# Kernel tuning notes

Hardware: AMD Instinct MI355X
Metric: run time of the kernel (lower is better)

Reference implementation:

```python
import jax, jax.numpy as jnp
import numpy as np

DN = ('NCHW', 'OIHW', 'NCHW')


def conv(x, w, s, p):
    return jax.lax.conv_general_dilated(x, w, (s, s), [(p, p), (p, p)], dimension_numbers=DN)


def batchnorm(x, g, b, eps=1e-5):
    # torch BatchNorm2d in training mode: biased batch stats over (N,H,W)
    mu = jnp.mean(x, (0, 2, 3), keepdims=True)
    var = jnp.var(x, (0, 2, 3), keepdims=True)
    return (x - mu) * jax.lax.rsqrt(var + eps) * g.reshape(1, -1, 1, 1) + b.reshape(1, -1, 1, 1)


def pconv(x, mask, W, b, s, p, gb, act):
    # PartialConvLayer.forward
    k = W.shape[-1]
    y = conv(x * mask, W, s, p)
    mc = conv(mask, jnp.ones((1, 1, k, k), x.dtype), s, p)  # all-ones mask conv (frozen)
    zero = mc == 0
    msum = jnp.where(zero, 1.0, mc)
    if b is not None:
        bias = b.reshape(1, -1, 1, 1)
        y = (y - bias) / msum + bias
    else:
        y = y / msum
    y = jnp.where(zero, 0.0, y)
    new_mask = jnp.where(zero, 0.0, 1.0).astype(x.dtype)
    if gb is not None:
        y = batchnorm(y, gb[0], gb[1])
    if act == 'relu':
        y = jax.nn.relu(y)
    elif act == 'leaky':
        y = jnp.where(y >= 0, y, 0.2 * y)
    return y, new_mask


def nlm(mask, feat, h2):
    # Vectorized batch_NLM: Nadaraya-Watson estimator between miss and bkg pixels.
    # Equivalent to the original triple loop: for each miss pixel i,
    #   out[i] = sum_j exp(-||x_i-x_j||^2/h^2) x_j / sum_j exp(-...)   over bkg j.
    # Subtracting the per-row min distance before exp is mathematically identical
    # (the factor cancels in the ratio) and numerically stable.
    bs, C, H, W = feat.shape
    N = H * W
    x = feat.transpose(0, 2, 3, 1).reshape(bs, N, C)
    bkg = mask.reshape(bs, N) > 0.5
    sq = jnp.sum(x * x, -1)  # [bs,N]
    D = jnp.maximum(sq[:, :, None] + sq[:, None, :] - 2.0 * jnp.einsum('bic,bjc->bij', x, x), 0.0)
    Dm = jnp.where(bkg[:, None, :], D, jnp.inf)
    dmin = jnp.min(Dm, -1, keepdims=True)
    w = jnp.where(bkg[:, None, :], jnp.exp(-(D - dmin) / h2), 0.0)
    avg = jnp.einsum('bij,bjc->bic', w, x) / jnp.sum(w, -1, keepdims=True)
    out = jnp.where(bkg[:, :, None], x, avg)  # only miss pixels are replaced
    return out.reshape(bs, H, W, C).transpose(0, 3, 1, 2)


def up2(x):
    return jnp.repeat(jnp.repeat(x, 2, axis=2), 2, axis=3)


def forward(input_x, mask, enc1_W, enc2_W, enc3_W, enc4_W, dec4_W, dec3_W, dec2_W, dec1_W, dec1_b,
            enc2_g, enc2_b, enc3_g, enc3_b, enc4_g, enc4_b,
            dec4_g, dec4_b, dec3_g, dec3_b, dec2_g, dec2_b):
    H_GAUSS2 = 25.0  # h_gaussian = 5
    h0, m0 = input_x, mask
    h1, m1 = pconv(h0, m0, enc1_W, None, 2, 3, None, 'relu')                 # down-7, bn=False
    h2, m2 = pconv(h1, m1, enc2_W, None, 2, 2, (enc2_g, enc2_b), 'relu')     # down-5
    # NLM feature swapping at layer 2 (torch code detaches -> stop_gradient)
    h2 = jax.lax.stop_gradient(nlm(m2, h2, H_GAUSS2))
    buffer_swapped = h2
    h3, m3 = pconv(h2, m2, enc3_W, None, 2, 1, (enc3_g, enc3_b), 'relu')     # down-3
    h4, m4 = pconv(h3, m3, enc4_W, None, 2, 1, (enc4_g, enc4_b), 'relu')     # down-3

    out, omask = h4, m4
    out, omask = up2(out), up2(omask)
    out, omask = pconv(jnp.concatenate([out, h3], 1), omask, dec4_W, None, 1, 1, (dec4_g, dec4_b), 'leaky')
    out, omask = up2(out), up2(omask)
    out, omask = pconv(jnp.concatenate([out, buffer_swapped], 1), omask, dec3_W, None, 1, 1, (dec3_g, dec3_b), 'leaky')
    out, omask = up2(out), up2(omask)
    out, omask = pconv(jnp.concatenate([out, h1], 1), omask, dec2_W, None, 1, 1, (dec2_g, dec2_b), 'leaky')
    out, omask = up2(out), up2(omask)
    out, omask = pconv(jnp.concatenate([out, h0], 1), omask, dec1_W, dec1_b, 1, 1, None, 'none')  # bn=False, bias, no act
    return out


def setup_inputs() -> dict:
    key = jax.random.key(0)
    ks = jax.random.split(key, 12)

    def kaiming(k, shape):
        fan_in = shape[1] * shape[2] * shape[3]
        return jax.random.normal(k, shape, jnp.float32) * np.float32(np.sqrt(2.0 / fan_in))

    bs = 8
    input_x = jax.random.normal(ks[0], (bs, 128, 144, 144), jnp.float32)
    # mask: 1 = background (valid), 0 = missing. Hole large enough to survive two downsamples.
    mask = jnp.ones((bs, 1, 144, 144), jnp.float32).at[:, :, 40:96, 40:96].set(0.0)

    inp = {
        'input_x': input_x,
        'mask': mask,
        'enc1_W': kaiming(ks[1], (256, 128, 7, 7)),
        'enc2_W': kaiming(ks[2], (512, 256, 5, 5)),
        'enc3_W': kaiming(ks[3], (512, 512, 3, 3)),
        'enc4_W': kaiming(ks[4], (512, 512, 3, 3)),
        'dec4_W': kaiming(ks[5], (512, 1024, 3, 3)),
        'dec3_W': kaiming(ks[6], (512, 1024, 3, 3)),
        'dec2_W': kaiming(ks[7], (256, 768, 3, 3)),
        'dec1_W': kaiming(ks[8], (128, 384, 3, 3)),
        'dec1_b': jnp.zeros((128,), jnp.float32),
    }
    for name, c in [('enc2', 512), ('enc3', 512), ('enc4', 512), ('dec4', 512), ('dec3', 512), ('dec2', 256)]:
        inp[name + '_g'] = jnp.ones((c,), jnp.float32)
        inp[name + '_b'] = jnp.zeros((c,), jnp.float32)
    return inp


def reference(input_x, mask, enc1_W, enc2_W, enc3_W, enc4_W, dec4_W, dec3_W, dec2_W, dec1_W, dec1_b,
              enc2_g, enc2_b, enc3_g, enc3_b, enc4_g, enc4_b,
              dec4_g, dec4_b, dec3_g, dec3_b, dec2_g, dec2_b):
    return forward(input_x, mask, enc1_W, enc2_W, enc3_W, enc4_W, dec4_W, dec3_W, dec2_W, dec1_W, dec1_b,
                   enc2_g, enc2_b, enc3_g, enc3_b, enc4_g, enc4_b,
                   dec4_g, dec4_b, dec3_g, dec3_b, dec2_g, dec2_b)
```

## Files before the change

kernel.cpp:

```cpp
#include <hip/hip_runtime.h>
#include <math.h>

#define ACT_NONE 0
#define ACT_RELU 1
#define ACT_LEAKY 2

#define EPI_F32 0
#define EPI_PAIR_RELU 1
#define EPI_F32_BIAS 2

typedef __attribute__((ext_vector_type(8))) short short8;
typedef __attribute__((ext_vector_type(8))) __bf16 bf16x8;
typedef __attribute__((ext_vector_type(4))) float f32x4;
typedef __attribute__((ext_vector_type(4))) unsigned uint4v;

__device__ __forceinline__ float actf(float y, int act) {
    if (act == ACT_RELU)  return y > 0.f ? y : 0.f;
    if (act == ACT_LEAKY) return y >= 0.f ? y : 0.2f * y;
    return y;
}

__device__ __forceinline__ unsigned f2bf_rne(float f) {
    unsigned u = __float_as_uint(f);
    return (u + 0x7FFFu + ((u >> 16) & 1u)) >> 16;
}
__device__ __forceinline__ float bf2f(unsigned h) { return __uint_as_float(h << 16); }
__device__ __forceinline__ unsigned splitpack(float f) {
    unsigned hi = f2bf_rne(f);
    float r = f - bf2f(hi);
    unsigned lo = f2bf_rne(r);
    return (hi & 0xFFFFu) | (lo << 16);
}

__device__ __forceinline__ f32x4 mfma16(short8 a, short8 b, f32x4 c) {
    return __builtin_amdgcn_mfma_f32_16x16x32_bf16(
        __builtin_bit_cast(bf16x8, a), __builtin_bit_cast(bf16x8, b), c, 0, 0, 0);
}

template<int K, int S, bool MHALF>
__global__ void maskconv_kernel(const float* __restrict__ M, int HM, int WM,
                                float* __restrict__ mc, float* __restrict__ nm,
                                int N, int Hin, int Win, int Hout, int Wout) {
    constexpr int P = (K - 1) / 2;
    int idx = blockIdx.x * blockDim.x + threadIdx.x;
    int total = N * Hout * Wout;
    if (idx >= total) return;
    int wo = idx % Wout;
    int t  = idx / Wout;
    int ho = t % Hout;
    int n  = t / Hout;
    float s = 0.f;
    for (int kh = 0; kh < K; ++kh) {
        int ih = ho * S - P + kh;
        if ((unsigned)ih >= (unsigned)Hin) continue;
        const float* mrow = M + ((size_t)n * HM + (MHALF ? (ih >> 1) : ih)) * WM;
        for (int kw = 0; kw < K; ++kw) {
            int iw = wo * S - P + kw;
            if ((unsigned)iw < (unsigned)Win)
                s += mrow[MHALF ? (iw >> 1) : iw];
// ... 7 lines not shown
                           short* __restrict__ Wlo, int Cout, int Cin, int Ksz,
                           size_t total) {
    size_t idx = (size_t)blockIdx.x * blockDim.x + threadIdx.x;
    if (idx >= total) return;
    int j = (int)(idx & 7);
    int lane = (int)((idx >> 3) & 63);
    size_t r = idx >> 9;
    int COB = Cout >> 4, KB = Cin >> 5;
    int cob = (int)(r % COB); r /= COB;
    int kb = (int)(r % KB);
    int tap = (int)(r / KB);
    int co = cob * 16 + (lane & 15);
    int ci = kb * 32 + (lane >> 4) * 8 + j;
    float f = W[((size_t)co * Cin + ci) * Ksz + tap];
    unsigned hi = f2bf_rne(f);
    float rr = f - bf2f(hi);
    unsigned lo = f2bf_rne(rr);
    Whi[idx] = (short)hi;
    Wlo[idx] = (short)lo;
}

template<int K, int S, int TH, int TW, int NFW, bool AF32, int EPI>
__global__ __launch_bounds__(512) void conv_enc(
    const void* __restrict__ Asrc, int Cin, int Hin, int Win,
    const float* __restrict__ M,
    const short* __restrict__ Whi, const short* __restrict__ Wlo,
    const float* __restrict__ mc, const float* __restrict__ bias,
    void* __restrict__ outp,
    int Hout, int Wout, int Cout, int TX)
{
    static_assert(S == 2, "parity layout assumes stride 2");
    constexpr int P = (K - 1) / 2;
    constexpr int HH  = (TH - 1) * S + K;
    constexpr int HWC = (TW - 1) * S + K;
    constexpr int PXC = HH * HWC;
    static_assert(PXC <= 512, "one halo pixel per thread");
    constexpr int PW  = (HWC + 1) / 2;
    constexpr int PXC2 = HH * PW * 2;
    __shared__ __align__(16) unsigned BH[4 * PXC2 * 4];
    __shared__ __align__(16) unsigned BL[4 * PXC2 * 4];

    const int t    = threadIdx.x;
    const int lane = t & 63;
    const int wv   = t >> 6;
    const int wm   = wv >> 1;
    const int wn   = wv & 1;
    const int img  = blockIdx.z;
    const int coB  = blockIdx.y * 256;
    const int tile = blockIdx.x;
    const int ty   = tile / TX, tx = tile - ty * TX;
    const int oy0  = ty * TH, ox0 = tx * TW;
    const int KB   = Cin >> 5;
    const int COB  = Cout >> 4;
    const size_t HW = (size_t)Hin * Win;
    const int g  = lane >> 4;
    const int pl = lane & 15;

    bool sel = false;
    size_t base = 0;
    int qq = 0;
    if (t < PXC) {
        const int r = t / HWC, c = t - r * HWC;
        qq = r * PW + (c >> 1) + (c & 1) * (HH * PW);
        const int iy = oy0 * S - P + r;
        const int ix = ox0 * S - P + c;
        if ((unsigned)iy < (unsigned)Hin && (unsigned)ix < (unsigned)Win) {
            if (M[(size_t)img * HW + (size_t)iy * Win + ix] != 0.f) {
                sel = true;
                base = (size_t)img * Cin * HW + (size_t)iy * Win + ix;
            }
        }
    }

    unsigned vr[4][8];
    auto prefetch = [&](int kb) {
#pragma unroll
        for (int gg = 0; gg < 4; ++gg) {
            const int c0 = kb * 32 + gg * 8;
#pragma unroll
            for (int j = 0; j < 8; ++j) vr[gg][j] = 0u;
            if (sel) {
                const unsigned* s = (const unsigned*)Asrc + base + (size_t)c0 * HW;
#pragma unroll
                for (int j = 0; j < 8; ++j) vr[gg][j] = s[(size_t)j * HW];
            }
        }
    };

    f32x4 acc[4][NFW] = {};
    if (t < PXC) prefetch(0);

#pragma unroll 1
    for (int kb = 0; kb < KB; ++kb) {
        if (t < PXC) {
#pragma unroll
            for (int gg = 0; gg < 4; ++gg) {
                unsigned v[8];
#pragma unroll
                for (int j = 0; j < 8; ++j) {
                    v[j] = vr[gg][j];
                    if (AF32) v[j] = splitpack(__uint_as_float(v[j]));
                }
                uint4v hd, ld;
#pragma unroll
                for (int j = 0; j < 4; ++j) {
                    hd[j] = (v[2 * j] & 0xFFFFu) | (v[2 * j + 1] << 16);
                    ld[j] = (v[2 * j] >> 16) | (v[2 * j + 1] & 0xFFFF0000u);
                }
                *(uint4v*)&BH[(gg * PXC2 + qq) * 4] = hd;
                *(uint4v*)&BL[(gg * PXC2 + qq) * 4] = ld;
            }
        }
        __syncthreads();
        if (t < PXC && kb + 1 < KB) prefetch(kb + 1);

#pragma unroll 1
        for (int kh = 0; kh < K; ++kh)
#pragma unroll 1
        for (int kw = 0; kw < K; ++kw) {
            const int tap = kh * K + kw;
            const size_t wb = (((size_t)tap * KB + kb) * COB + (coB >> 4) + wm * 4) * 512
                            + (size_t)lane * 8;
            short8 ah[4], al[4];
#pragma unroll
            for (int fm = 0; fm < 4; ++fm) {
                ah[fm] = *(const short8*)(Whi + wb + (size_t)fm * 512);
                al[fm] = *(const short8*)(Wlo + wb + (size_t)fm * 512);
            }
#pragma unroll
            for (int fn = 0; fn < NFW; ++fn) {
                const int pxf = (wn * NFW + fn) * 16 + pl;
                const int oy = pxf / TW, ox = pxf - oy * TW;
                const int q2 = (oy * S + kh) * PW + ox + (kw >> 1) + (kw & 1) * (HH * PW);
                short8 bh = *(const short8*)&BH[(g * PXC2 + q2) * 4];
                short8 bl = *(const short8*)&BL[(g * PXC2 + q2) * 4];
#pragma unroll
                for (int fm = 0; fm < 4; ++fm) {
                    acc[fm][fn] = mfma16(ah[fm], bh, acc[fm][fn]);
                    acc[fm][fn] = mfma16(al[fm], bh, acc[fm][fn]);
                    acc[fm][fn] = mfma16(ah[fm], bl, acc[fm][fn]);
                }
            }
        }
        __syncthreads();
    }

    const int Npix = Hout * Wout;
    const float* mcb = mc + (size_t)img * Npix;
#pragma unroll
    for (int fm = 0; fm < 4; ++fm)
#pragma unroll
    for (int fn = 0; fn < NFW; ++fn) {
        const int co = coB + (wm * 4 + fm) * 16 + (lane >> 4) * 4;
        const int pxf = (wn * NFW + fn) * 16 + (lane & 15);
        const int oy = pxf / TW, ox = pxf - oy * TW;
        const int gy = oy0 + oy, gx = ox0 + ox;
        if (gy >= Hout || gx >= Wout) continue;
        const float m = mcb[(size_t)gy * Wout + gx];
        f32x4 a = acc[fm][fn];
#pragma unroll
        for (int r = 0; r < 4; ++r) {
            float y = a[r];
            if (EPI == EPI_F32_BIAS) {
                const float bv = bias[co + r];
                y = (m == 0.f) ? 0.f : (y - bv) / m + bv;
            } else {
                y = (m == 0.f) ? 0.f : y / m;
            }
            const size_t oidx = ((size_t)img * Cout + co + r) * Npix + (size_t)gy * Wout + gx;
            if (EPI == EPI_PAIR_RELU) {
                y = y > 0.f ? y : 0.f;
                ((unsigned*)outp)[oidx] = splitpack(y);
            } else {
                ((float*)outp)[oidx] = y;
            }
        }
    }
}

template<int TH, int TW, int NFW, bool BF32, int EPI>
__global__ __launch_bounds__(512) void conv3x3(
    const void* __restrict__ Asrc, int CA, int HA, int WA,
    const void* __restrict__ Bsrc, int CB,
    const float* __restrict__ M,
    const short* __restrict__ Whi, const short* __restrict__ Wlo,
    const float* __restrict__ mc, const float* __restrict__ bias,
    void* __restrict__ outp,
    int Hout, int Wout, int Cout, int TX)
{
    constexpr int HALO_H = TH + 2, HALO_W = TW + 2, HALO = HALO_H * HALO_W;
    constexpr int NPIX = TH * TW;
    constexpr int SITER = (HALO + 127) / 128;
    static_assert(NPIX == 32 * NFW, "tile must be exactly 32*NFW pixels");
    __shared__ __align__(16) unsigned BH[4 * HALO * 4];
    __shared__ __align__(16) unsigned BL[4 * HALO * 4];

    const int t    = threadIdx.x;
    const int lane = t & 63;
    const int wv   = t >> 6;
    const int wm   = wv >> 1;
    const int wn   = wv & 1;
    const int img  = blockIdx.z;
    const int coB  = blockIdx.y * 128;
    const int tile = blockIdx.x;
    const int ty   = tile / TX;
    const int tx   = tile - ty * TX;
    const int oy0  = ty * TH, ox0 = tx * TW;
    const int Cin  = CA + CB;
    const int KB   = Cin >> 5;
    const int COB  = Cout >> 4;
    const int WM   = Wout >> 1;
    const size_t HWA = (size_t)HA * WA;
    const size_t HWB = (size_t)Hout * Wout;

    const int sg = t >> 7;
    const int st = t & 127;
    const int g  = lane >> 4;
    const int pl = lane & 15;

    bool ssel[SITER];
    size_t sA[SITER], sB[SITER];
#pragma unroll
    for (int i = 0; i < SITER; ++i) {
        ssel[i] = false; sA[i] = 0; sB[i] = 0;
        const int q = st + i * 128;
        if (q < HALO) {
            const int hy = q / HALO_W, hx = q - hy * HALO_W;
            const int iy = oy0 - 1 + hy, ix = ox0 - 1 + hx;
            if ((unsigned)iy < (unsigned)Hout && (unsigned)ix < (unsigned)Wout) {
                if (M[((size_t)img * (Hout >> 1) + (iy >> 1)) * WM + (ix >> 1)] != 0.f) {
                    ssel[i] = true;
                    sA[i] = (size_t)img * CA * HWA + (size_t)(iy >> 1) * WA + (ix >> 1);
                    sB[i] = (size_t)img * CB * HWB + (size_t)iy * Wout + ix;
                }
            }
        }
    }

    unsigned vr[SITER][8];
    auto prefetch = [&](int kb) {
        const int c = kb * 32 + sg * 8;
#pragma unroll
        for (int i = 0; i < SITER; ++i) {
            const int q = st + i * 128;
#pragma unroll
            for (int j = 0; j < 8; ++j) vr[i][j] = 0u;
            if (q < HALO && ssel[i]) {
                if (c < CA) {
                    const unsigned* s = (const unsigned*)Asrc + sA[i] + (size_t)c * HWA;
#pragma unroll
                    for (int j = 0; j < 8; ++j) vr[i][j] = s[(size_t)j * HWA];
                } else {
                    const unsigned* s = (const unsigned*)Bsrc + sB[i] + (size_t)(c - CA) * HWB;
#pragma unroll
                    for (int j = 0; j < 8; ++j) vr[i][j] = s[(size_t)j * HWB];
                }
            }
        }
    };

    f32x4 acc[2][NFW] = {};
    const size_t wstride = (size_t)KB * COB * 512;
    prefetch(0);

#pragma unroll 1
    for (int kb = 0; kb < KB; ++kb) {
        const bool isB = (kb * 32 + sg * 8) >= CA;
#pragma unroll
        for (int i = 0; i < SITER; ++i) {
            const int q = st + i * 128;
            if (q < HALO) {
                unsigned v[8];
#pragma unroll
                for (int j = 0; j < 8; ++j) {
                    v[j] = vr[i][j];
                    if (BF32 && isB) v[j] = splitpack(__uint_as_float(v[j]));
                }
                uint4v hd, ld;
#pragma unroll
                for (int j = 0; j < 4; ++j) {
                    hd[j] = (v[2 * j] & 0xFFFFu) | (v[2 * j + 1] << 16);
                    ld[j] = (v[2 * j] >> 16) | (v[2 * j + 1] & 0xFFFF0000u);
                }
                *(uint4v*)&BH[(sg * HALO + q) * 4] = hd;
                *(uint4v*)&BL[(sg * HALO + q) * 4] = ld;
            }
        }
        __syncthreads();
        if (kb + 1 < KB) prefetch(kb + 1);

        size_t wb = ((size_t)kb * COB + (coB >> 4) + wm * 2) * 512 + (size_t)lane * 8;
#pragma unroll 1
        for (int tap = 0; tap < 9; ++tap) {
            const int dh = tap / 3, dw = tap - dh * 3;
            short8 ah0 = *(const short8*)(Whi + wb);
            short8 ah1 = *(const short8*)(Whi + wb + 512);
            short8 al0 = *(const short8*)(Wlo + wb);
            short8 al1 = *(const short8*)(Wlo + wb + 512);
#pragma unroll
            for (int fn = 0; fn < NFW; ++fn) {
                const int pxf = (wn * NFW + fn) * 16 + pl;
                const int oy = pxf / TW, ox = pxf - oy * TW;
                const int hpx = (oy + dh) * HALO_W + (ox + dw);
                short8 bh = *(const short8*)&BH[(g * HALO + hpx) * 4];
                short8 bl = *(const short8*)&BL[(g * HALO + hpx) * 4];
                acc[0][fn] = mfma16(ah0, bh, acc[0][fn]);
                acc[1][fn] = mfma16(ah1, bh, acc[1][fn]);
                acc[0][fn] = mfma16(al0, bh, acc[0][fn]);
                acc[1][fn] = mfma16(al1, bh, acc[1][fn]);
                acc[0][fn] = mfma16(ah0, bl, acc[0][fn]);
                acc[1][fn] = mfma16(ah1, bl, acc[1][fn]);
            }
            wb += wstride;
        }
        __syncthreads();
    }

    const float* mcb = mc + (size_t)img * HWB;
#pragma unroll
    for (int fm = 0; fm < 2; ++fm)
#pragma unroll
    for (int fn = 0; fn < NFW; ++fn) {
        const int co = coB + (wm * 2 + fm) * 16 + (lane >> 4) * 4;
        const int pxf = (wn * NFW + fn) * 16 + (lane & 15);
        const int oy = pxf / TW, ox = pxf - oy * TW;
        const int gy = oy0 + oy, gx = ox0 + ox;
        if (gy >= Hout || gx >= Wout) continue;
        const float m = mcb[(size_t)gy * Wout + gx];
// ... 20 lines not shown
    double s = 0.0, s2 = 0.0;
    const int tot = N * HW;
    for (int i = threadIdx.x; i < tot; i += blockDim.x) {
        int n = i / HW, hw = i - n * HW;
        float v = y[((size_t)n * C + c) * HW + hw];
        s += v;
        s2 += (double)v * v;
    }
    __shared__ double sh[256], sh2[256];
    sh[threadIdx.x] = s; sh2[threadIdx.x] = s2;
    __syncthreads();
    for (int o = 128; o > 0; o >>= 1) {
        if (threadIdx.x < o) { sh[threadIdx.x] += sh[threadIdx.x + o]; sh2[threadIdx.x] += sh2[threadIdx.x + o]; }
        __syncthreads();
    }
    if (threadIdx.x == 0) {
        double mu = sh[0] / tot;
        double var = sh2[0] / tot - mu * mu;
        mean[c] = (float)mu;
        istd[c] = (float)(1.0 / sqrt(var + 1e-5));
    }
}

__global__ void bn_apply_pair(const float* __restrict__ y,
                              const float* __restrict__ mean, const float* __restrict__ istd,
                              const float* __restrict__ g, const float* __restrict__ b,
                              unsigned* __restrict__ pout, float* __restrict__ fout,
                              int C, int HW, int total, int act) {
    int idx = blockIdx.x * blockDim.x + threadIdx.x;
    if (idx >= total) return;
    int c = (idx / HW) % C;
    float v = (y[idx] - mean[c]) * istd[c] * g[c] + b[c];
    v = actf(v, act);
    pout[idx] = splitpack(v);
    if (fout) fout[idx] = v;
}

#define NLM_C 512
#define NLM_N 1296
#define NLM_MAXM 256
#define NLM_RT 16
#define NLM_KB1 16
#define NLM_KB2 41
#define NLM_PFRAG (NLM_KB1 * NLM_RT * 512)
#define NLM_WFRAG (NLM_KB2 * NLM_RT * 512)

__global__ __launch_bounds__(256) void nlm_trans(const float* __restrict__ h2f,
                                                 unsigned* __restrict__ xTp) {
    __shared__ float tile[32][33];
    const int b = blockIdx.z;
    const int j0 = blockIdx.x * 32, c0 = blockIdx.y * 32;
    const int tx = threadIdx.x & 31, ty = threadIdx.x >> 5;
    for (int cc = ty; cc < 32; cc += 8) {
        const int j = j0 + tx;
        tile[cc][tx] = (j < NLM_N) ? h2f[((size_t)b * NLM_C + c0 + cc) * NLM_N + j] : 0.f;
    }
    __syncthreads();
    for (int jj = ty; jj < 32; jj += 8) {
// ... 166 lines not shown
            lsum += w;
        }
        const unsigned u = splitpack(w);
        const int kb = j >> 5, kg = (j & 31) >> 3, jj = j & 7;
        const int lane = kg * 16 + lr;
        const size_t f = (size_t)img * NLM_WFRAG
                       + ((size_t)(kb * NLM_RT + rt) * 64 + lane) * 8 + jj;
        W2hi[f] = (short)(u & 0xFFFFu);
        W2lo[f] = (short)(u >> 16);
    }
    red[tid] = lsum;
    __syncthreads();
    for (int o = 128; o > 0; o >>= 1) {
        if (tid < o) red[tid] += red[tid + o];
        __syncthreads();
    }
    if (tid == 0) sumw[img * NLM_MAXM + i] = red[0];
}

__global__ __launch_bounds__(512) void nlm_gemm2(
    const unsigned* __restrict__ xTp, const short* __restrict__ W2hi,
    const short* __restrict__ W2lo, const int* __restrict__ cnt,
    const float* __restrict__ sumw, const int* __restrict__ list,
    unsigned* __restrict__ out) {
    const int img = blockIdx.z, mt = blockIdx.y, ct = blockIdx.x;
    const int cN = cnt[img] < NLM_MAXM ? cnt[img] : NLM_MAXM;
    if (mt * 128 >= cN) return;
    __shared__ __align__(16) unsigned BH[4 * 128 * 4];
    __shared__ __align__(16) unsigned BL[4 * 128 * 4];
    const int t = threadIdx.x, lane = t & 63, wv = t >> 6, wm = wv >> 1, wn = wv & 1;
    const int c0 = ct * 128;
    const int sc = t & 127, sg = t >> 7;
    f32x4 acc[2][4] = {};
#pragma unroll 1
    for (int kb = 0; kb < NLM_KB2; ++kb) {
        unsigned v[8];
#pragma unroll
        for (int jj = 0; jj < 8; ++jj) {
            const int j = kb * 32 + sg * 8 + jj;
            v[jj] = (j < NLM_N)
                  ? xTp[((size_t)img * NLM_N + j) * NLM_C + c0 + sc] : 0u;
        }
        uint4v hd, ld;
#pragma unroll
        for (int jj = 0; jj < 4; ++jj) {
            hd[jj] = (v[2 * jj] & 0xFFFFu) | (v[2 * jj + 1] << 16);
            ld[jj] = (v[2 * jj] >> 16) | (v[2 * jj + 1] & 0xFFFF0000u);
// ... 14 lines not shown
            short8 bh = *(const short8*)&BH[(g * 128 + px) * 4];
            short8 bl = *(const short8*)&BL[(g * 128 + px) * 4];
            acc[0][fn] = mfma16(ah0, bh, acc[0][fn]);
            acc[1][fn] = mfma16(ah1, bh, acc[1][fn]);
            acc[0][fn] = mfma16(al0, bh, acc[0][fn]);
            acc[1][fn] = mfma16(al1, bh, acc[1][fn]);
            acc[0][fn] = mfma16(ah0, bl, acc[0][fn]);
            acc[1][fn] = mfma16(ah1, bl, acc[1][fn]);
        }
        __syncthreads();
    }
#pragma unroll
    for (int fm = 0; fm < 2; ++fm)
#pragma unroll
    for (int fn = 0; fn < 4; ++fn) {
        const int row = mt * 128 + (wm * 2 + fm) * 16 + (lane >> 4) * 4;
        const int c = c0 + wn * 64 + fn * 16 + (lane & 15);
        f32x4 a = acc[fm][fn];
#pragma unroll
        for (int r = 0; r < 4; ++r) {
            const int ri = row + r;
            if (ri < cN) {
                const float y = a[r] / sumw[img * NLM_MAXM + ri];
                out[((size_t)img * NLM_C + c) * NLM_N + list[img * NLM_MAXM + ri]]
                    = splitpack(y);
            }
        }
    }
}

extern "C" void kernel_launch(void* const* d_in, const int* in_sizes, int n_in,
                              void* d_out, int out_size, void* d_ws, size_t ws_size,
                              hipStream_t stream) {
    const float* x0    = (const float*)d_in[0];
    const float* m0    = (const float*)d_in[1];
    const float* Wsrc[8] = {
        (const float*)d_in[2], (const float*)d_in[3], (const float*)d_in[4],
        (const float*)d_in[5], (const float*)d_in[6], (const float*)d_in[7],
        (const float*)d_in[8], (const float*)d_in[9]
    };
    const float* dec1b = (const float*)d_in[10];
    const float* enc2g = (const float*)d_in[11];
    const float* enc2b = (const float*)d_in[12];
    const float* enc3g = (const float*)d_in[13];
    const float* enc3b = (const float*)d_in[14];
    const float* enc4g = (const float*)d_in[15];
    const float* enc4b = (const float*)d_in[16];
    const float* dec4g = (const float*)d_in[17];
    const float* dec4b = (const float*)d_in[18];
    const float* dec3g = (const float*)d_in[19];
    const float* dec3b = (const float*)d_in[20];
    const float* dec2g = (const float*)d_in[21];
    const float* dec2b = (const float*)d_in[22];
    float* outp = (float*)d_out;

    const int N = 8;
    float* ws = (float*)d_ws;
    size_t off = 0;
    auto alloc = [&](size_t nf) {
        size_t o = off;
        off += ((nf + 63) / 64) * 64;
        return ws + o;
    };

    unsigned* h1pair  = (unsigned*)alloc(10616832);
    unsigned* h2spair = (unsigned*)alloc(5308416);
    unsigned* h3pair  = (unsigned*)alloc(1327104);
    unsigned* h4pair  = (unsigned*)alloc(331776);
    unsigned* d4pair  = (unsigned*)alloc(1327104);
    float* ybuf = alloc(10616832);
    float* h2f  = alloc(5308416);
    unsigned* xTp = (unsigned*)alloc(5308416);
    float* sqb  = alloc(10368);
    float* mc   = alloc(165888);
    float* nm1  = alloc(41472);
    float* nm2  = alloc(10368);
    float* nm3  = alloc(2592);
    float* nm4  = alloc(648);
    float* nmd4 = alloc(2592);
    float* nmd3 = alloc(10368);
    float* nmd2 = alloc(41472);
    float* nmx  = alloc(165888);
    float* bmean = alloc(512);
    float* bistd = alloc(512);
    short* Whi = (short*)alloc(10625024);
    short* Wlo = (short*)alloc(10625024);
    float* Smat = alloc((size_t)8 * NLM_MAXM * NLM_N);
    short* Phi  = (short*)alloc((size_t)8 * NLM_PFRAG / 2);
    short* Plo  = (short*)alloc((size_t)8 * NLM_PFRAG / 2);
    short* W2hi = (short*)alloc((size_t)8 * NLM_WFRAG / 2);
    short* W2lo = (short*)alloc((size_t)8 * NLM_WFRAG / 2);
    int*   mlist = (int*)alloc(8 * NLM_MAXM);
    int*   mcnt  = (int*)alloc(64);
    float* sumw  = alloc(8 * NLM_MAXM);
    unsigned* d3pair = h2spair;
    unsigned* d2pair = h1pair;

    if (ws_size < off * sizeof(float)) return;

    auto cdiv = [](size_t a, size_t b) { return (int)((a + b - 1) / b); };

    struct WLay { int Cout, Cin, K; size_t ofs; };
    const WLay WL[8] = {
        {256, 128, 7, 0},
        {512, 256, 5, 1605632},
        {512, 512, 3, 4882432},
        {512, 512, 3, 7241728},
        {512, 1024, 3, 9601024},
        {512, 1024, 3, 14319616},
        {256, 768, 3, 19038208},
        {128, 384, 3, 20807680},
    };
    for (int i = 0; i < 8; ++i) {
        size_t tot = (size_t)WL[i].Cout * WL[i].Cin * WL[i].K * WL[i].K;
        wtransform<<<cdiv(tot, 256), 256, 0, stream>>>(
            Wsrc[i], Whi + WL[i].ofs, Wlo + WL[i].ofs, WL[i].Cout, WL[i].Cin,
            WL[i].K * WL[i].K, tot);
    }

    maskconv_kernel<7, 2, false><<<cdiv(N * 72 * 72, 256), 256, 0, stream>>>(
        m0, 144, 144, mc, nm1, N, 144, 144, 72, 72);
    conv_enc<7, 2, 8, 8, 2, true, EPI_PAIR_RELU><<<dim3(81, 1, N), 512, 0, stream>>>(
        x0, 128, 144, 144, m0,
        Whi + WL[0].ofs, Wlo + WL[0].ofs, mc, nullptr, h1pair,
        72, 72, 256, 9);

    maskconv_kernel<5, 2, false><<<cdiv(N * 36 * 36, 256), 256, 0, stream>>>(
        nm1, 72, 72, mc, nm2, N, 72, 72, 36, 36);
    conv_enc<5, 2, 8, 8, 2, false, EPI_F32><<<dim3(25, 2, N), 512, 0, stream>>>(
        h1pair, 256, 72, 72, nm1,
        Whi + WL[1].ofs, Wlo + WL[1].ofs, mc, nullptr, ybuf,
        36, 36, 512, 5);
    bn_stats_kernel<<<512, 256, 0, stream>>>(ybuf, N, 512, 1296, bmean, bistd);
    bn_apply_pair<<<cdiv(5308416, 256), 256, 0, stream>>>(
        ybuf, bmean, bistd, enc2g, enc2b, h2spair, h2f, 512, 1296, 5308416, ACT_RELU);

    nlm_trans<<<dim3(41, 16, N), 256, 0, stream>>>(h2f, xTp);
    nlm_sq2<<<dim3(6, N), 256, 0, stream>>>(h2f, sqb);
    hipMemsetAsync(mcnt, 0, 8 * sizeof(int), stream);
    nlm_compact<<<N, 256, 0, stream>>>(nm2, mlist, mcnt);
    nlm_gather<<<dim3(64, N), 256, 0, stream>>>(xTp, mlist, mcnt, Phi, Plo);
    nlm_gemm1<<<dim3(11, 2, N), 512, 0, stream>>>(xTp, Phi, Plo, mcnt, Smat);
    nlm_row<<<dim3(NLM_MAXM, N), 256, 0, stream>>>(Smat, sqb, nm2, mlist, mcnt,
                                                   W2hi, W2lo, sumw, 1.f / 25.f);
    nlm_gemm2<<<dim3(4, 2, N), 512, 0, stream>>>(xTp, W2hi, W2lo, mcnt, sumw,
                                                 mlist, h2spair);

    maskconv_kernel<3, 2, false><<<cdiv(N * 18 * 18, 256), 256, 0, stream>>>(
        nm2, 36, 36, mc, nm3, N, 36, 36, 18, 18);
    conv_enc<3, 2, 4, 8, 1, false, EPI_F32><<<dim3(15, 2, N), 512, 0, stream>>>(
        h2spair, 512, 36, 36, nm2,
        Whi + WL[2].ofs, Wlo + WL[2].ofs, mc, nullptr, ybuf,
        18, 18, 512, 3);
    bn_stats_kernel<<<512, 256, 0, stream>>>(ybuf, N, 512, 324, bmean, bistd);
    bn_apply_pair<<<cdiv(1327104, 256), 256, 0, stream>>>(
        ybuf, bmean, bistd, enc3g, enc3b, h3pair, nullptr, 512, 324, 1327104, ACT_RELU);

    maskconv_kernel<3, 2, false><<<cdiv(N * 9 * 9, 256), 256, 0, stream>>>(
        nm3, 18, 18, mc, nm4, N, 18, 18, 9, 9);
    conv_enc<3, 2, 4, 8, 1, false, EPI_F32><<<dim3(6, 2, N), 512, 0, stream>>>(
        h3pair, 512, 18, 18, nm3,
        Whi + WL[3].ofs, Wlo + WL[3].ofs, mc, nullptr, ybuf,
        9, 9, 512, 2);
    bn_stats_kernel<<<512, 256, 0, stream>>>(ybuf, N, 512, 81, bmean, bistd);
    bn_apply_pair<<<cdiv(331776, 256), 256, 0, stream>>>(
        ybuf, bmean, bistd, enc4g, enc4b, h4pair, nullptr, 512, 81, 331776, ACT_RELU);

    maskconv_kernel<3, 1, true><<<cdiv(N * 18 * 18, 256), 256, 0, stream>>>(
        nm4, 9, 9, mc, nmd4, N, 18, 18, 18, 18);
    conv3x3<8, 8, 2, false, EPI_F32><<<dim3(9, 4, N), 512, 0, stream>>>(
        h4pair, 512, 9, 9, h3pair, 512, nm4,
        Whi + WL[4].ofs, Wlo + WL[4].ofs, mc, nullptr, ybuf,
        18, 18, 512, 3);
    bn_stats_kernel<<<512, 256, 0, stream>>>(ybuf, N, 512, 324, bmean, bistd);
    bn_apply_pair<<<cdiv(1327104, 256), 256, 0, stream>>>(
        ybuf, bmean, bistd, dec4g, dec4b, d4pair, nullptr, 512, 324, 1327104, ACT_LEAKY);

    maskconv_kernel<3, 1, true><<<cdiv(N * 36 * 36, 256), 256, 0, stream>>>(
        nmd4, 18, 18, mc, nmd3, N, 36, 36, 36, 36);
    conv3x3<8, 12, 3, false, EPI_F32><<<dim3(15, 4, N), 512, 0, stream>>>(
        d4pair, 512, 18, 18, h2spair, 512, nmd4,
        Whi + WL[5].ofs, Wlo + WL[5].ofs, mc, nullptr, ybuf,
        36, 36, 512, 3);
    bn_stats_kernel<<<512, 256, 0, stream>>>(ybuf, N, 512, 1296, bmean, bistd);
    bn_apply_pair<<<cdiv(5308416, 256), 256, 0, stream>>>(
        ybuf, bmean, bistd, dec3g, dec3b, d3pair, nullptr, 512, 1296, 5308416, ACT_LEAKY);

    maskconv_kernel<3, 1, true><<<cdiv(N * 72 * 72, 256), 256, 0, stream>>>(
        nmd3, 36, 36, mc, nmd2, N, 72, 72, 72, 72);
    conv3x3<8, 16, 4, false, EPI_F32><<<dim3(45, 2, N), 512, 0, stream>>>(
        d3pair, 512, 36, 36, h1pair, 256, nmd3,
        Whi + WL[6].ofs, Wlo + WL[6].ofs, mc, nullptr, ybuf,
        72, 72, 256, 5);
    bn_stats_kernel<<<256, 256, 0, stream>>>(ybuf, N, 256, 5184, bmean, bistd);
    bn_apply_pair<<<cdiv(10616832, 256), 256, 0, stream>>>(
        ybuf, bmean, bistd, dec2g, dec2b, d2pair, nullptr, 256, 5184, 10616832, ACT_LEAKY);

    maskconv_kernel<3, 1, true><<<cdiv(N * 144 * 144, 256), 256, 0, stream>>>(
        nmd2, 72, 72, mc, nmx, N, 144, 144, 144, 144);
    conv3x3<8, 16, 4, true, EPI_F32_BIAS><<<dim3(162, 1, N), 512, 0, stream>>>(
        d2pair, 256, 72, 72, x0, 128, nmd2,
        Whi + WL[7].ofs, Wlo + WL[7].ofs, mc, dec1b, outp,
        144, 144, 128, 9);
}
```

Baseline: 2.826 ms.

## Store split-bf16 activations in channel-blocked planar hi/lo layout for vector loads

Intermediate activations change from interleaved hi/lo 32-bit pairs in NCHW order to separate hi and lo bf16 planes laid out as [img][C/32][pixel][32]. The conv kernels can then fetch eight channels per pixel with one 16-byte load instead of eight strided scalar loads, and no longer need to repack before writing LDS. LDS rows are padded to reduce bank conflicts. The BN-apply kernel becomes a tiled transpose that writes the new layout, and the NLM and enc1 epilogues now emit the same layout through scattered 16-bit stores.

```diff
diff --git a/kernel.cpp b/kernel.cpp
--- a/kernel.cpp
+++ b/kernel.cpp
@@ -35,6 +35,10 @@
 __device__ __forceinline__ f32x4 mfma16(short8 a, short8 b, f32x4 c) {
     return __builtin_amdgcn_mfma_f32_16x16x32_bf16(
         __builtin_bit_cast(bf16x8, a), __builtin_bit_cast(bf16x8, b), c, 0, 0, 0);
+}
+
+__device__ __forceinline__ size_t paddr(int img, int KBc, size_t HW, size_t pix) {
+    return ((size_t)img * KBc * HW + pix) * 32;
 }
 
 template<int K, int S, bool MHALF>
@@ -88,11 +92,12 @@
 
 template<int K, int S, int TH, int TW, int NFW, bool AF32, int EPI>
 __global__ __launch_bounds__(512) void conv_enc(
-    const void* __restrict__ Asrc, int Cin, int Hin, int Win,
+    const void* __restrict__ Ahi, const void* __restrict__ Alo,
+    int Cin, int Hin, int Win,
     const float* __restrict__ M,
     const short* __restrict__ Whi, const short* __restrict__ Wlo,
     const float* __restrict__ mc, const float* __restrict__ bias,
-    void* __restrict__ outp,
+    void* __restrict__ outp, void* __restrict__ outp2,
     int Hout, int Wout, int Cout, int TX)
 {
     static_assert(S == 2, "parity layout assumes stride 2");
@@ -103,8 +108,9 @@
     static_assert(PXC <= 512, "one halo pixel per thread");
     constexpr int PW  = (HWC + 1) / 2;
     constexpr int PXC2 = HH * PW * 2;
-    __shared__ __align__(16) unsigned BH[4 * PXC2 * 4];
-    __shared__ __align__(16) unsigned BL[4 * PXC2 * 4];
+    constexpr int PXC2P = PXC2 + ((2 - (PXC2 % 8) + 8) % 8);
+    __shared__ __align__(16) short BHs[4 * PXC2P * 8];
+    __shared__ __align__(16) short BLs[4 * PXC2P * 8];
 
     const int t    = threadIdx.x;
     const int lane = t & 63;
@@ -123,7 +129,7 @@
     const int pl = lane & 15;
 
     bool sel = false;
-    size_t base = 0;
+    size_t basef = 0, basep = 0;
     int qq = 0;
     if (t < PXC) {
         const int r = t / HWC, c = t - r * HWC;
@@ -131,24 +137,38 @@
         const int iy = oy0 * S - P + r;
         const int ix = ox0 * S - P + c;
         if ((unsigned)iy < (unsigned)Hin && (unsigned)ix < (unsigned)Win) {
-            if (M[(size_t)img * HW + (size_t)iy * Win + ix] != 0.f) {
+            const size_t pix = (size_t)iy * Win + ix;
+            if (M[(size_t)img * HW + pix] != 0.f) {
                 sel = true;
-                base = (size_t)img * Cin * HW + (size_t)iy * Win + ix;
-            }
-        }
-    }
-
-    unsigned vr[4][8];
+                basef = (size_t)img * Cin * HW + pix;
+                basep = paddr(img, KB, HW, pix);
+            }
+        }
+    }
+
+    short8 hv[4], lv[4];
     auto prefetch = [&](int kb) {
 #pragma unroll
         for (int gg = 0; gg < 4; ++gg) {
-            const int c0 = kb * 32 + gg * 8;
-#pragma unroll
-            for (int j = 0; j < 8; ++j) vr[gg][j] = 0u;
             if (sel) {
-                const unsigned* s = (const unsigned*)Asrc + base + (size_t)c0 * HW;
-#pragma unroll
-                for (int j = 0; j < 8; ++j) vr[gg][j] = s[(size_t)j * HW];
+                if (AF32) {
+                    const float* s = (const float*)Ahi + basef + (size_t)(kb * 32 + gg * 8) * HW;
+#pragma unroll
+                    for (int j = 0; j < 8; ++j) {
+                        float f = s[(size_t)j * HW];
+                        unsigned h16 = f2bf_rne(f);
+                        float rr = f - bf2f(h16);
+                        hv[gg][j] = (short)h16;
+                        lv[gg][j] = (short)f2bf_rne(rr);
+                    }
+                } else {
+                    const size_t a = basep + (size_t)kb * HW * 32 + gg * 8;
+                    hv[gg] = *(const short8*)((const short*)Ahi + a);
+                    lv[gg] = *(const short8*)((const short*)Alo + a);
+                }
+            } else {
+#pragma unroll
+                for (int j = 0; j < 8; ++j) { hv[gg][j] = 0; lv[gg][j] = 0; }
             }
         }
     };
@@ -161,20 +181,8 @@
         if (t < PXC) {
 #pragma unroll
             for (int gg = 0; gg < 4; ++gg) {
-                unsigned v[8];
-#pragma unroll
-                for (int j = 0; j < 8; ++j) {
-                    v[j] = vr[gg][j];
-                    if (AF32) v[j] = splitpack(__uint_as_float(v[j]));
-                }
-                uint4v hd, ld;
-#pragma unroll
-                for (int j = 0; j < 4; ++j) {
-                    hd[j] = (v[2 * j] & 0xFFFFu) | (v[2 * j + 1] << 16);
-                    ld[j] = (v[2 * j] >> 16) | (v[2 * j + 1] & 0xFFFF0000u);
-                }
-                *(uint4v*)&BH[(gg * PXC2 + qq) * 4] = hd;
-                *(uint4v*)&BL[(gg * PXC2 + qq) * 4] = ld;
+                *(short8*)&BHs[(gg * PXC2P + qq) * 8] = hv[gg];
+                *(short8*)&BLs[(gg * PXC2P + qq) * 8] = lv[gg];
             }
         }
         __syncthreads();
@@ -198,8 +206,8 @@
                 const int pxf = (wn * NFW + fn) * 16 + pl;
                 const int oy = pxf / TW, ox = pxf - oy * TW;
                 const int q2 = (oy * S + kh) * PW + ox + (kw >> 1) + (kw & 1) * (HH * PW);
-                short8 bh = *(const short8*)&BH[(g * PXC2 + q2) * 4];
-                short8 bl = *(const short8*)&BL[(g * PXC2 + q2) * 4];
+                short8 bh = *(const short8*)&BHs[(g * PXC2P + q2) * 8];
+                short8 bl = *(const short8*)&BLs[(g * PXC2P + q2) * 8];
 #pragma unroll
                 for (int fm = 0; fm < 4; ++fm) {
                     acc[fm][fn] = mfma16(ah[fm], bh, acc[fm][fn]);
@@ -222,7 +230,8 @@
         const int oy = pxf / TW, ox = pxf - oy * TW;
         const int gy = oy0 + oy, gx = ox0 + ox;
         if (gy >= Hout || gx >= Wout) continue;
-        const float m = mcb[(size_t)gy * Wout + gx];
+        const size_t pix = (size_t)gy * Wout + gx;
+        const float m = mcb[pix];
         f32x4 a = acc[fm][fn];
 #pragma unroll
         for (int r = 0; r < 4; ++r) {
@@ -233,12 +242,16 @@
             } else {
                 y = (m == 0.f) ? 0.f : y / m;
             }
-            const size_t oidx = ((size_t)img * Cout + co + r) * Npix + (size_t)gy * Wout + gx;
             if (EPI == EPI_PAIR_RELU) {
                 y = y > 0.f ? y : 0.f;
-                ((unsigned*)outp)[oidx] = splitpack(y);
+                const size_t pa = paddr(img, Cout >> 5, Npix, pix)
+                                + (size_t)(co >> 5) * Npix * 32 + (co & 31) + r;
+                unsigned h16 = f2bf_rne(y);
+                float rr = y - bf2f(h16);
+                ((short*)outp)[pa]  = (short)h16;
+                ((short*)outp2)[pa] = (short)f2bf_rne(rr);
             } else {
-                ((float*)outp)[oidx] = y;
+                ((float*)outp)[((size_t)img * Cout + co + r) * Npix + pix] = y;
             }
         }
     }
@@ -246,8 +259,9 @@
 
 template<int TH, int TW, int NFW, bool BF32, int EPI>
 __global__ __launch_bounds__(512) void conv3x3(
-    const void* __restrict__ Asrc, int CA, int HA, int WA,
-    const void* __restrict__ Bsrc, int CB,
+    const void* __restrict__ Ahi, const void* __restrict__ Alo,
+    int CA, int HA, int WA,
+    const void* __restrict__ Bhi, const void* __restrict__ Blo, int CB,
     const float* __restrict__ M,
     const short* __restrict__ Whi, const short* __restrict__ Wlo,
     const float* __restrict__ mc, const float* __restrict__ bias,
@@ -255,11 +269,12 @@
     int Hout, int Wout, int Cout, int TX)
 {
     constexpr int HALO_H = TH + 2, HALO_W = TW + 2, HALO = HALO_H * HALO_W;
+    constexpr int HALOP = HALO + ((2 - (HALO % 8) + 8) % 8);
     constexpr int NPIX = TH * TW;
     constexpr int SITER = (HALO + 127) / 128;
     static_assert(NPIX == 32 * NFW, "tile must be exactly 32*NFW pixels");
-    __shared__ __align__(16) unsigned BH[4 * HALO * 4];
-    __shared__ __align__(16) unsigned BL[4 * HALO * 4];
+    __shared__ __align__(16) short BHs[4 * HALOP * 8];
+    __shared__ __align__(16) short BLs[4 * HALOP * 8];
 
     const int t    = threadIdx.x;
     const int lane = t & 63;
@@ -274,6 +289,8 @@
     const int oy0  = ty * TH, ox0 = tx * TW;
     const int Cin  = CA + CB;
     const int KB   = Cin >> 5;
+    const int KBA  = CA >> 5;
+    const int KBB  = CB >> 5;
     const int COB  = Cout >> 4;
     const int WM   = Wout >> 1;
     const size_t HWA = (size_t)HA * WA;
@@ -285,10 +302,10 @@
     const int pl = lane & 15;
 
     bool ssel[SITER];
-    size_t sA[SITER], sB[SITER];
+    size_t aoff[SITER], boff[SITER];
 #pragma unroll
     for (int i = 0; i < SITER; ++i) {
-        ssel[i] = false; sA[i] = 0; sB[i] = 0;
+        ssel[i] = false; aoff[i] = 0; boff[i] = 0;
         const int q = st + i * 128;
         if (q < HALO) {
             const int hy = q / HALO_W, hx = q - hy * HALO_W;
@@ -296,31 +313,48 @@
             if ((unsigned)iy < (unsigned)Hout && (unsigned)ix < (unsigned)Wout) {
                 if (M[((size_t)img * (Hout >> 1) + (iy >> 1)) * WM + (ix >> 1)] != 0.f) {
                     ssel[i] = true;
-                    sA[i] = (size_t)img * CA * HWA + (size_t)(iy >> 1) * WA + (ix >> 1);
-                    sB[i] = (size_t)img * CB * HWB + (size_t)iy * Wout + ix;
+                    const size_t pixA = (size_t)(iy >> 1) * WA + (ix >> 1);
+                    const size_t pixB = (size_t)iy * Wout + ix;
+                    aoff[i] = paddr(img, KBA, HWA, pixA) + sg * 8;
+                    if (BF32) boff[i] = (size_t)img * CB * HWB + pixB;
+                    else      boff[i] = paddr(img, KBB, HWB, pixB) + sg * 8;
                 }
             }
         }
     }
 
-    unsigned vr[SITER][8];
+    short8 hv[SITER], lv[SITER];
     auto prefetch = [&](int kb) {
         const int c = kb * 32 + sg * 8;
 #pragma unroll
         for (int i = 0; i < SITER; ++i) {
             const int q = st + i * 128;
-#pragma unroll
-            for (int j = 0; j < 8; ++j) vr[i][j] = 0u;
-            if (q < HALO && ssel[i]) {
+            bool ok = (q < HALO) && ssel[i];
+            if (ok) {
                 if (c < CA) {
-                    const unsigned* s = (const unsigned*)Asrc + sA[i] + (size_t)c * HWA;
-#pragma unroll
-                    for (int j = 0; j < 8; ++j) vr[i][j] = s[(size_t)j * HWA];
+                    const size_t a = aoff[i] + (size_t)kb * HWA * 32;
+                    hv[i] = *(const short8*)((const short*)Ahi + a);
+                    lv[i] = *(const short8*)((const short*)Alo + a);
                 } else {
-                    const unsigned* s = (const unsigned*)Bsrc + sB[i] + (size_t)(c - CA) * HWB;
-#pragma unroll
-                    for (int j = 0; j < 8; ++j) vr[i][j] = s[(size_t)j * HWB];
+                    if (BF32) {
+                        const float* s = (const float*)Bhi + boff[i] + (size_t)(c - CA) * HWB;
+#pragma unroll
+                        for (int j = 0; j < 8; ++j) {
+                            float f = s[(size_t)j * HWB];
+                            unsigned h16 = f2bf_rne(f);
+                            float rr = f - bf2f(h16);
+                            hv[i][j] = (short)h16;
+                            lv[i][j] = (short)f2bf_rne(rr);
+                        }
+                    } else {
+                        const size_t a = boff[i] + (size_t)(kb - KBA) * HWB * 32;
+                        hv[i] = *(const short8*)((const short*)Bhi + a);
+                        lv[i] = *(const short8*)((const short*)Blo + a);
+                    }
                 }
+            } else {
+#pragma unroll
+                for (int j = 0; j < 8; ++j) { hv[i][j] = 0; lv[i][j] = 0; }
             }
         }
     };
@@ -331,31 +365,18 @@
 
 #pragma unroll 1
     for (int kb = 0; kb < KB; ++kb) {
-        const bool isB = (kb * 32 + sg * 8) >= CA;
 #pragma unroll
         for (int i = 0; i < SITER; ++i) {
             const int q = st + i * 128;
             if (q < HALO) {
-                unsigned v[8];
-#pragma unroll
-                for (int j = 0; j < 8; ++j) {
-                    v[j] = vr[i][j];
-                    if (BF32 && isB) v[j] = splitpack(__uint_as_float(v[j]));
-                }
-                uint4v hd, ld;
-#pragma unroll
-                for (int j = 0; j < 4; ++j) {
-                    hd[j] = (v[2 * j] & 0xFFFFu) | (v[2 * j + 1] << 16);
-                    ld[j] = (v[2 * j] >> 16) | (v[2 * j + 1] & 0xFFFF0000u);
-                }
-                *(uint4v*)&BH[(sg * HALO + q) * 4] = hd;
-                *(uint4v*)&BL[(sg * HALO + q) * 4] = ld;
+                *(short8*)&BHs[(sg * HALOP + q) * 8] = hv[i];
+                *(short8*)&BLs[(sg * HALOP + q) * 8] = lv[i];
             }
         }
         __syncthreads();
         if (kb + 1 < KB) prefetch(kb + 1);
 
-        size_t wb = ((size_t)kb * COB + (coB >> 4) + wm * 2) * 512 + (size_t)lane * 8;
+        size_t wb = ((size_t)kb * COB + (coB >> 4) + wm * 2) * 512 + lane * 8;
 #pragma unroll 1
         for (int tap = 0; tap < 9; ++tap) {
             const int dh = tap / 3, dw = tap - dh * 3;
@@ -368,8 +389,8 @@
                 const int pxf = (wn * NFW + fn) * 16 + pl;
                 const int oy = pxf / TW, ox = pxf - oy * TW;
                 const int hpx = (oy + dh) * HALO_W + (ox + dw);
-                short8 bh = *(const short8*)&BH[(g * HALO + hpx) * 4];
-                short8 bl = *(const short8*)&BL[(g * HALO + hpx) * 4];
+                short8 bh = *(const short8*)&BHs[(g * HALOP + hpx) * 8];
+                short8 bl = *(const short8*)&BLs[(g * HALOP + hpx) * 8];
                 acc[0][fn] = mfma16(ah0, bh, acc[0][fn]);
                 acc[1][fn] = mfma16(ah1, bh, acc[1][fn]);
                 acc[0][fn] = mfma16(al0, bh, acc[0][fn]);
@@ -436,18 +457,52 @@
     }
 }
 
-__global__ void bn_apply_pair(const float* __restrict__ y,
-                              const float* __restrict__ mean, const float* __restrict__ istd,
-                              const float* __restrict__ g, const float* __restrict__ b,
-                              unsigned* __restrict__ pout, float* __restrict__ fout,
-                              int C, int HW, int total, int act) {
-    int idx = blockIdx.x * blockDim.x + threadIdx.x;
-    if (idx >= total) return;
-    int c = (idx / HW) % C;
-    float v = (y[idx] - mean[c]) * istd[c] * g[c] + b[c];
-    v = actf(v, act);
-    pout[idx] = splitpack(v);
-    if (fout) fout[idx] = v;
+__global__ __launch_bounds__(256) void bn_apply_blk(
+    const float* __restrict__ y,
+    const float* __restrict__ mean, const float* __restrict__ istd,
+    const float* __restrict__ g, const float* __restrict__ b,
+    short* __restrict__ hi, short* __restrict__ lo, float* __restrict__ fout,
+    int C, int HW, int act) {
+    __shared__ float tile[32][65];
+    const int img = blockIdx.z, kb = blockIdx.y;
+    const int px0 = blockIdx.x * 64;
+    const int tid = threadIdx.x;
+    const int KBc = C >> 5;
+
+    for (int i = tid; i < 32 * 64; i += 256) {
+        const int ch = i >> 6, px = i & 63;
+        float v = 0.f;
+        if (px0 + px < HW)
+            v = y[((size_t)img * C + kb * 32 + ch) * HW + px0 + px];
+        tile[ch][px] = v;
+    }
+    __syncthreads();
+
+    const int px = tid >> 2, sg = tid & 3;
+    if (px0 + px < HW) {
+        short8 h8, l8;
+        float f8[8];
+#pragma unroll
+        for (int j = 0; j < 8; ++j) {
+            const int c = kb * 32 + sg * 8 + j;
+            float v = tile[sg * 8 + j][px];
+            v = (v - mean[c]) * istd[c] * g[c] + b[c];
+            v = actf(v, act);
+            f8[j] = v;
+            unsigned h16 = f2bf_rne(v);
+            float rr = v - bf2f(h16);
+            h8[j] = (short)h16;
+            l8[j] = (short)f2bf_rne(rr);
+        }
+        const size_t a = (((size_t)img * KBc + kb) * HW + px0 + px) * 32 + sg * 8;
+        *(short8*)&hi[a] = h8;
+        *(short8*)&lo[a] = l8;
+        if (fout) {
+#pragma unroll
+            for (int j = 0; j < 8; ++j)
+                fout[((size_t)img * C + kb * 32 + sg * 8 + j) * HW + px0 + px] = f8[j];
+        }
+    }
 }
 
 #define NLM_C 512
@@ -660,7 +715,7 @@
     const unsigned* __restrict__ xTp, const short* __restrict__ W2hi,
     const short* __restrict__ W2lo, const int* __restrict__ cnt,
     const float* __restrict__ sumw, const int* __restrict__ list,
-    unsigned* __restrict__ out) {
+    short* __restrict__ outHi, short* __restrict__ outLo) {
     const int img = blockIdx.z, mt = blockIdx.y, ct = blockIdx.x;
     const int cN = cnt[img] < NLM_MAXM ? cnt[img] : NLM_MAXM;
     if (mt * 128 >= cN) return;
@@ -721,8 +776,13 @@
             const int ri = row + r;
             if (ri < cN) {
                 const float y = a[r] / sumw[img * NLM_MAXM + ri];
-                out[((size_t)img * NLM_C + c) * NLM_N + list[img * NLM_MAXM + ri]]
-                    = splitpack(y);
+                const int pix = list[img * NLM_MAXM + ri];
+                const size_t pa = (((size_t)img * (NLM_C >> 5) + (c >> 5)) * NLM_N + pix) * 32
+                                + (c & 31);
+                unsigned h16 = f2bf_rne(y);
+                float rr = y - bf2f(h16);
+                outHi[pa] = (short)h16;
+                outLo[pa] = (short)f2bf_rne(rr);
             }
         }
     }
@@ -761,12 +821,18 @@
         off += ((nf + 63) / 64) * 64;
         return ws + o;
     };
-
-    unsigned* h1pair  = (unsigned*)alloc(10616832);
-    unsigned* h2spair = (unsigned*)alloc(5308416);
-    unsigned* h3pair  = (unsigned*)alloc(1327104);
-    unsigned* h4pair  = (unsigned*)alloc(331776);
-    unsigned* d4pair  = (unsigned*)alloc(1327104);
+    auto allocPair = [&](size_t E, short** hi, short** lo) {
+        float* p = alloc(E);
+        *hi = (short*)p;
+        *lo = (short*)p + E;
+    };
+
+    short *h1hi, *h1lo, *h2shi, *h2slo, *h3hi, *h3lo, *h4hi, *h4lo, *d4hi, *d4lo;
+    allocPair(10616832, &h1hi, &h1lo);
+    allocPair(5308416, &h2shi, &h2slo);
+    allocPair(1327104, &h3hi, &h3lo);
+    allocPair(331776, &h4hi, &h4lo);
+    allocPair(1327104, &d4hi, &d4lo);
     float* ybuf = alloc(10616832);
     float* h2f  = alloc(5308416);
     unsigned* xTp = (unsigned*)alloc(5308416);
@@ -785,15 +851,17 @@
     short* Whi = (short*)alloc(10625024);
     short* Wlo = (short*)alloc(10625024);
     float* Smat = alloc((size_t)8 * NLM_MAXM * NLM_N);
-    short* Phi  = (short*)alloc((size_t)8 * NLM_PFRAG / 2);
-    short* Plo  = (short*)alloc((size_t)8 * NLM_PFRAG / 2);
-    short* W2hi = (short*)alloc((size_t)8 * NLM_WFRAG / 2);
-    short* W2lo = (short*)alloc((size_t)8 * NLM_WFRAG / 2);
+    float* Phi_  = alloc((size_t)8 * NLM_PFRAG / 2);
+    float* Plo_  = alloc((size_t)8 * NLM_PFRAG / 2);
+    float* W2hi_ = alloc((size_t)8 * NLM_WFRAG / 2);
+    float* W2lo_ = alloc((size_t)8 * NLM_WFRAG / 2);
+    short* Phi = (short*)Phi_;  short* Plo = (short*)Plo_;
+    short* W2hi = (short*)W2hi_; short* W2lo = (short*)W2lo_;
     int*   mlist = (int*)alloc(8 * NLM_MAXM);
     int*   mcnt  = (int*)alloc(64);
     float* sumw  = alloc(8 * NLM_MAXM);
-    unsigned* d3pair = h2spair;
-    unsigned* d2pair = h1pair;
+    short* d3hi = h2shi; short* d3lo = h2slo;
+    short* d2hi = h1hi;  short* d2lo = h1lo;
 
     if (ws_size < off * sizeof(float)) return;
 
@@ -820,19 +888,19 @@
     maskconv_kernel<7, 2, false><<<cdiv(N * 72 * 72, 256), 256, 0, stream>>>(
         m0, 144, 144, mc, nm1, N, 144, 144, 72, 72);
     conv_enc<7, 2, 8, 8, 2, true, EPI_PAIR_RELU><<<dim3(81, 1, N), 512, 0, stream>>>(
-        x0, 128, 144, 144, m0,
-        Whi + WL[0].ofs, Wlo + WL[0].ofs, mc, nullptr, h1pair,
+        x0, nullptr, 128, 144, 144, m0,
+        Whi + WL[0].ofs, Wlo + WL[0].ofs, mc, nullptr, h1hi, h1lo,
         72, 72, 256, 9);
 
     maskconv_kernel<5, 2, false><<<cdiv(N * 36 * 36, 256), 256, 0, stream>>>(
         nm1, 72, 72, mc, nm2, N, 72, 72, 36, 36);
     conv_enc<5, 2, 8, 8, 2, false, EPI_F32><<<dim3(25, 2, N), 512, 0, stream>>>(
-        h1pair, 256, 72, 72, nm1,
-        Whi + WL[1].ofs, Wlo + WL[1].ofs, mc, nullptr, ybuf,
+        h1hi, h1lo, 256, 72, 72, nm1,
+        Whi + WL[1].ofs, Wlo + WL[1].ofs, mc, nullptr, ybuf, nullptr,
         36, 36, 512, 5);
     bn_stats_kernel<<<512, 256, 0, stream>>>(ybuf, N, 512, 1296, bmean, bistd);
-    bn_apply_pair<<<cdiv(5308416, 256), 256, 0, stream>>>(
-        ybuf, bmean, bistd, enc2g, enc2b, h2spair, h2f, 512, 1296, 5308416, ACT_RELU);
+    bn_apply_blk<<<dim3(cdiv(1296, 64), 16, N), 256, 0, stream>>>(
+        ybuf, bmean, bistd, enc2g, enc2b, h2shi, h2slo, h2f, 512, 1296, ACT_RELU);
 
     nlm_trans<<<dim3(41, 16, N), 256, 0, stream>>>(h2f, xTp);
     nlm_sq2<<<dim3(6, N), 256, 0, stream>>>(h2f, sqb);
@@ -843,62 +911,62 @@
     nlm_row<<<dim3(NLM_MAXM, N), 256, 0, stream>>>(Smat, sqb, nm2, mlist, mcnt,
                                                    W2hi, W2lo, sumw, 1.f / 25.f);
     nlm_gemm2<<<dim3(4, 2, N), 512, 0, stream>>>(xTp, W2hi, W2lo, mcnt, sumw,
-                                                 mlist, h2spair);
+                                                 mlist, h2shi, h2slo);
 
     maskconv_kernel<3, 2, false><<<cdiv(N * 18 * 18, 256), 256, 0, stream>>>(
         nm2, 36, 36, mc, nm3, N, 36, 36, 18, 18);
     conv_enc<3, 2, 4, 8, 1, false, EPI_F32><<<dim3(15, 2, N), 512, 0, stream>>>(
-        h2spair, 512, 36, 36, nm2,
-        Whi + WL[2].ofs, Wlo + WL[2].ofs, mc, nullptr, ybuf,
+        h2shi, h2slo, 512, 36, 36, nm2,
+        Whi + WL[2].ofs, Wlo + WL[2].ofs, mc, nullptr, ybuf, nullptr,
         18, 18, 512, 3);
     bn_stats_kernel<<<512, 256, 0, stream>>>(ybuf, N, 512, 324, bmean, bistd);
-    bn_apply_pair<<<cdiv(1327104, 256), 256, 0, stream>>>(
-        ybuf, bmean, bistd, enc3g, enc3b, h3pair, nullptr, 512, 324, 1327104, ACT_RELU);
+    bn_apply_blk<<<dim3(cdiv(324, 64), 16, N), 256, 0, stream>>>(
+        ybuf, bmean, bistd, enc3g, enc3b, h3hi, h3lo, nullptr, 512, 324, ACT_RELU);
 
     maskconv_kernel<3, 2, false><<<cdiv(N * 9 * 9, 256), 256, 0, stream>>>(
         nm3, 18, 18, mc, nm4, N, 18, 18, 9, 9);
     conv_enc<3, 2, 4, 8, 1, false, EPI_F32><<<dim3(6, 2, N), 512, 0, stream>>>(
-        h3pair, 512, 18, 18, nm3,
-        Whi + WL[3].ofs, Wlo + WL[3].ofs, mc, nullptr, ybuf,
+        h3hi, h3lo, 512, 18, 18, nm3,
+        Whi + WL[3].ofs, Wlo + WL[3].ofs, mc, nullptr, ybuf, nullptr,
         9, 9, 512, 2);
     bn_stats_kernel<<<512, 256, 0, stream>>>(ybuf, N, 512, 81, bmean, bistd);
-    bn_apply_pair<<<cdiv(331776, 256), 256, 0, stream>>>(
-        ybuf, bmean, bistd, enc4g, enc4b, h4pair, nullptr, 512, 81, 331776, ACT_RELU);
+    bn_apply_blk<<<dim3(cdiv(81, 64), 16, N), 256, 0, stream>>>(
+        ybuf, bmean, bistd, enc4g, enc4b, h4hi, h4lo, nullptr, 512, 81, ACT_RELU);
 
     maskconv_kernel<3, 1, true><<<cdiv(N * 18 * 18, 256), 256, 0, stream>>>(
         nm4, 9, 9, mc, nmd4, N, 18, 18, 18, 18);
     conv3x3<8, 8, 2, false, EPI_F32><<<dim3(9, 4, N), 512, 0, stream>>>(
-        h4pair, 512, 9, 9, h3pair, 512, nm4,
+        h4hi, h4lo, 512, 9, 9, h3hi, h3lo, 512, nm4,
         Whi + WL[4].ofs, Wlo + WL[4].ofs, mc, nullptr, ybuf,
         18, 18, 512, 3);
     bn_stats_kernel<<<512, 256, 0, stream>>>(ybuf, N, 512, 324, bmean, bistd);
-    bn_apply_pair<<<cdiv(1327104, 256), 256, 0, stream>>>(
-        ybuf, bmean, bistd, dec4g, dec4b, d4pair, nullptr, 512, 324, 1327104, ACT_LEAKY);
+    bn_apply_blk<<<dim3(cdiv(324, 64), 16, N), 256, 0, stream>>>(
+        ybuf, bmean, bistd, dec4g, dec4b, d4hi, d4lo, nullptr, 512, 324, ACT_LEAKY);
 
     maskconv_kernel<3, 1, true><<<cdiv(N * 36 * 36, 256), 256, 0, stream>>>(
         nmd4, 18, 18, mc, nmd3, N, 36, 36, 36, 36);
     conv3x3<8, 12, 3, false, EPI_F32><<<dim3(15, 4, N), 512, 0, stream>>>(
-        d4pair, 512, 18, 18, h2spair, 512, nmd4,
+        d4hi, d4lo, 512, 18, 18, h2shi, h2slo, 512, nmd4,
         Whi + WL[5].ofs, Wlo + WL[5].ofs, mc, nullptr, ybuf,
         36, 36, 512, 3);
     bn_stats_kernel<<<512, 256, 0, stream>>>(ybuf, N, 512, 1296, bmean, bistd);
-    bn_apply_pair<<<cdiv(5308416, 256), 256, 0, stream>>>(
-        ybuf, bmean, bistd, dec3g, dec3b, d3pair, nullptr, 512, 1296, 5308416, ACT_LEAKY);
+    bn_apply_blk<<<dim3(cdiv(1296, 64), 16, N), 256, 0, stream>>>(
+        ybuf, bmean, bistd, dec3g, dec3b, d3hi, d3lo, nullptr, 512, 1296, ACT_LEAKY);
 
     maskconv_kernel<3, 1, true><<<cdiv(N * 72 * 72, 256), 256, 0, stream>>>(
         nmd3, 36, 36, mc, nmd2, N, 72, 72, 72, 72);
     conv3x3<8, 16, 4, false, EPI_F32><<<dim3(45, 2, N), 512, 0, stream>>>(
-        d3pair, 512, 36, 36, h1pair, 256, nmd3,
+        d3hi, d3lo, 512, 36, 36, h1hi, h1lo, 256, nmd3,
         Whi + WL[6].ofs, Wlo + WL[6].ofs, mc, nullptr, ybuf,
         72, 72, 256, 5);
     bn_stats_kernel<<<256, 256, 0, stream>>>(ybuf, N, 256, 5184, bmean, bistd);
-    bn_apply_pair<<<cdiv(10616832, 256), 256, 0, stream>>>(
-        ybuf, bmean, bistd, dec2g, dec2b, d2pair, nullptr, 256, 5184, 10616832, ACT_LEAKY);
+    bn_apply_blk<<<dim3(cdiv(5184, 64), 8, N), 256, 0, stream>>>(
+        ybuf, bmean, bistd, dec2g, dec2b, d2hi, d2lo, nullptr, 256, 5184, ACT_LEAKY);
 
     maskconv_kernel<3, 1, true><<<cdiv(N * 144 * 144, 256), 256, 0, stream>>>(
         nmd2, 72, 72, mc, nmx, N, 144, 144, 144, 144);
     conv3x3<8, 16, 4, true, EPI_F32_BIAS><<<dim3(162, 1, N), 512, 0, stream>>>(
-        d2pair, 256, 72, 72, x0, 128, nmd2,
+        d2hi, d2lo, 256, 72, 72, x0, nullptr, 128, nmd2,
         Whi + WL[7].ofs, Wlo + WL[7].ofs, mc, dec1b, outp,
         144, 144, 128, 9);
 }
```

After: 2.780 ms. No clear change (-1.6%).
